# Kernel optimization log

Measured on AMD Instinct MI355X. Metric: run time of the kernel, lower is better.

Reference implementation:

```python
import jax, jax.numpy as jnp
import numpy as np

B, C, D_MODEL, N_HEADS = 2, 2048, 1024, 16


def rotary_matrix(context_length: int, d: int) -> jnp.ndarray:
    """Faithful vectorization of get_rotary_matrix: theta = 10000^(-2*(i-1)/d)."""
    half = d // 2
    i = jnp.arange(half, dtype=jnp.float32)
    theta = 10000.0 ** (-2.0 * (i - 1.0) / d)          # note the (i-1), as in source
    m = jnp.arange(context_length, dtype=jnp.float32)
    ang = m[:, None] * theta                            # [C, d/2]
    c, s = jnp.cos(ang), jnp.sin(ang)
    ev = 2 * jnp.arange(half)
    od = ev + 1
    R = jnp.zeros((context_length, d, d), jnp.float32)
    R = R.at[:, ev, ev].set(c)
    R = R.at[:, ev, od].set(-s)
    R = R.at[:, od, ev].set(s)
    R = R.at[:, od, od].set(c)
    return R


def setup_inputs() -> dict:
    key = jax.random.key(0)
    k1, k2, k3, k4 = jax.random.split(key, 4)
    x = jax.random.normal(k1, (B, C, D_MODEL), dtype=jnp.float32)
    w_qkv = jax.random.normal(k2, (3 * D_MODEL, D_MODEL), dtype=jnp.float32) * 0.02
    w_out = jax.random.normal(k3, (D_MODEL, D_MODEL), dtype=jnp.float32) * 0.02
    b_out = jax.random.normal(k4, (D_MODEL,), dtype=jnp.float32) * 0.02
    return {"x": x, "w_qkv": w_qkv, "w_out": w_out, "b_out": b_out}


def reference(x, w_qkv, w_out, b_out):
    b, c, d = x.shape
    h = N_HEADS
    dh = d // h
    qkv = x @ w_qkv.T                                   # [B,C,3D]
    q, k, v = jnp.split(qkv, 3, axis=-1)
    # [B,C,D] -> [B,H,C,dh]
    q = q.reshape(b, c, h, dh).transpose(0, 2, 1, 3)
    k = k.reshape(b, c, h, dh).transpose(0, 2, 1, 3)
    v = v.reshape(b, c, h, dh).transpose(0, 2, 1, 3)
    R = rotary_matrix(c, dh)                            # [C,dh,dh]
    q_rot = jnp.einsum('bhci,cij->bhcj', q, R)
    k_rot = jnp.einsum('bhci,cij->bhcj', k, R)
    scale = jnp.sqrt(jnp.float32(dh))
    # exact math of the source: exp with no max subtraction, separate num/den
    attn_num = jnp.exp(jnp.einsum('bhqd,bhkd->bhqk', q_rot, k_rot) / scale)
    attn_den = jnp.exp(jnp.einsum('bhqd,bhkd->bhqk', q, k) / scale)
    attn_den = jnp.sum(attn_den, axis=-1, keepdims=True)
    attn = attn_num / attn_den
    causal = jnp.tril(jnp.ones((c, c), jnp.float32))[None, None]
    attn = jnp.where(causal == 0, 0.0, attn)
    y = jnp.einsum('bhqk,bhkd->bhqd', attn, v)
    y = y.transpose(0, 2, 1, 3).reshape(b, c, d)
    return y @ w_out.T + b_out
```

## Files before the change

kernel.cpp:

```cpp
#include <hip/hip_runtime.h>
#include <math.h>
#include <stdint.h>

#define BB 2
#define CC 2048
#define DD 1024
#define HH 16
#define DHH 64
#define HALF 32

typedef __attribute__((ext_vector_type(8))) short bf16x8;
typedef __attribute__((ext_vector_type(4))) float f32x4;
typedef unsigned int u32;

#define EXPC 0.1803368801f

__device__ __forceinline__ ushort f2bf(float f) {
    uint32_t u = __builtin_bit_cast(uint32_t, f);
    u = (u + 0x7FFFu + ((u >> 16) & 1u)) >> 16;
    return (ushort)u;
}

__device__ __forceinline__ void gload16(const void* g, void* lds) {
    __builtin_amdgcn_global_load_lds(
        (const u32 __attribute__((address_space(1)))*)g,
        (u32 __attribute__((address_space(3)))*)lds, 16, 0, 0);
}

__global__ __launch_bounds__(256) void cast3_k(const float* __restrict__ x,
                                               const float* __restrict__ wq,
                                               const float* __restrict__ wo,
                                               ushort* __restrict__ xb,
                                               ushort* __restrict__ wqb,
                                               ushort* __restrict__ wob) {
    int id = blockIdx.x * 256 + threadIdx.x;
    const float* s;
    ushort* d;
    int off;
    if (id < 524288)       { s = x;  d = xb;  off = id; }
    else if (id < 917504)  { s = wq; d = wqb; off = id - 524288; }
    else                   { s = wo; d = wob; off = id - 917504; }
    float4 a = *reinterpret_cast<const float4*>(s + (size_t)off * 8);
    float4 b = *reinterpret_cast<const float4*>(s + (size_t)off * 8 + 4);
    bf16x8 o;
    o[0] = (short)f2bf(a.x); o[1] = (short)f2bf(a.y);
    o[2] = (short)f2bf(a.z); o[3] = (short)f2bf(a.w);
    o[4] = (short)f2bf(b.x); o[5] = (short)f2bf(b.y);
    o[6] = (short)f2bf(b.z); o[7] = (short)f2bf(b.w);
    *reinterpret_cast<bf16x8*>(d + (size_t)off * 8) = o;
}

__global__ __launch_bounds__(256) void rope_table_k(float* __restrict__ ct, float* __restrict__ st) {
    int idx = blockIdx.x * 256 + threadIdx.x;
    if (idx >= CC * HALF) return;
    int m = idx >> 5;
    int t = idx & 31;
    double theta_d = pow(10000.0, -2.0 * ((double)t - 1.0) / 64.0);
    float theta = (float)theta_d;
    float ang = (float)m * theta;
    ct[idx] = cosf(ang);
    st[idx] = sinf(ang);
}

__global__ __launch_bounds__(256) void qkv_gemm_mfma_k(const ushort* __restrict__ xb,
                                                       const ushort* __restrict__ wqb,
                                                       const float* __restrict__ ct,
                                                       const float* __restrict__ st,
                                                       ushort* __restrict__ q,
                                                       ushort* __restrict__ k,
                                                       ushort* __restrict__ qr,
                                                       ushort* __restrict__ kr,
                                                       ushort* __restrict__ vT3) {
    __shared__ ushort Al[128 * 64];
    __shared__ ushort Bl[128 * 64];
    const int tid = threadIdx.x;
    const int w = tid >> 6, l = tid & 63;
    const int l15 = l & 15, lg = l >> 4;
    const int wr = w >> 1, wc = w & 1;
    const int m0 = blockIdx.x * 128, n0 = blockIdx.y * 128;
    const int lrow = l >> 3, lch = l & 7;

    f32x4 acc[4][4];
#pragma unroll
    for (int i = 0; i < 4; i++)
#pragma unroll
        for (int j = 0; j < 4; j++) acc[i][j] = (f32x4){0.f, 0.f, 0.f, 0.f};

    for (int k0 = 0; k0 < 1024; k0 += 64) {
        __syncthreads();
#pragma unroll
        for (int c = 0; c < 4; c++) {
            int row = w * 32 + c * 8 + lrow;
            int gch = (lch ^ (row & 7)) * 8;
            gload16(xb + (size_t)(m0 + row) * 1024 + k0 + gch, &Al[(w * 32 + c * 8) * 64]);
            gload16(wqb + (size_t)(n0 + row) * 1024 + k0 + gch, &Bl[(w * 32 + c * 8) * 64]);
        }
        __syncthreads();
#pragma unroll
        for (int kk = 0; kk < 2; kk++) {
            bf16x8 a[4], b[4];
#pragma unroll
            for (int mt = 0; mt < 4; mt++) {
                int row = wr * 64 + mt * 16 + l15;
                a[mt] = *reinterpret_cast<const bf16x8*>(&Al[row * 64 + ((kk * 4 + lg) ^ (row & 7)) * 8]);
            }
#pragma unroll
            for (int nt = 0; nt < 4; nt++) {
                int row = wc * 64 + nt * 16 + l15;
                b[nt] = *reinterpret_cast<const bf16x8*>(&Bl[row * 64 + ((kk * 4 + lg) ^ (row & 7)) * 8]);
            }
#pragma unroll
            for (int mt = 0; mt < 4; mt++)
#pragma unroll
                for (int nt = 0; nt < 4; nt++)
                    acc[mt][nt] = __builtin_amdgcn_mfma_f32_16x16x32_bf16(a[mt], b[nt], acc[mt][nt], 0, 0, 0);
        }
    }
#pragma unroll
    for (int mt = 0; mt < 4; mt++)
#pragma unroll
        for (int nt = 0; nt < 4; nt++) {
            int n = n0 + wc * 64 + nt * 16 + l15;
            int part = n >> 10;
            int d = n & 1023;
            int h = d >> 6, dd = d & 63;
            int mbase = m0 + wr * 64 + mt * 16 + lg * 4;
            int bb = mbase >> 11, cpos = mbase & 2047;
            if (part == 2) {
                int kt = cpos >> 6, kcol = cpos & 63;
                ushort4 pk;
                pk.x = f2bf(acc[mt][nt][0]); pk.y = f2bf(acc[mt][nt][1]);
                pk.z = f2bf(acc[mt][nt][2]); pk.w = f2bf(acc[mt][nt][3]);
                size_t off = ((((size_t)(bb * HH + h)) * 32 + kt) * 64 + dd) * 64 + kcol;
                *reinterpret_cast<ushort4*>(vT3 + off) = pk;
            } else {
                ushort* dstu = (part == 0) ? q : k;
                ushort* dstr = (part == 0) ? qr : kr;
                const float sgn = (dd & 1) ? -1.f : 1.f;
                const int t = dd >> 1;
#pragma unroll
                for (int r = 0; r < 4; r++) {
                    float val = acc[mt][nt][r];
                    float par = __shfl_xor(val, 1, 64);
                    float c = ct[(cpos + r) * 32 + t];
                    float s = st[(cpos + r) * 32 + t];
                    float rot = val * c + sgn * par * s;
                    size_t base = (((size_t)bb * HH + h) * CC + (cpos + r)) * DHH + dd;
                    dstu[base] = f2bf(val);
                    dstr[base] = f2bf(rot);
                }
            }
        }
}

__global__ __launch_bounds__(256, 2) void attn_fused_k(const ushort* __restrict__ vT3,
                                                       const ushort* __restrict__ qg,
                                                       const ushort* __restrict__ kg,
                                                       const ushort* __restrict__ qrg,
                                                       const ushort* __restrict__ krg,
                                                       ushort* __restrict__ y) {
    __shared__ ushort Kl[2][64 * 64];
    __shared__ ushort Krl[2][64 * 64];
    __shared__ ushort PlA[4][16 * 64];
    __shared__ ushort PlB[4][16 * 64];

    const int tid = threadIdx.x;
    const int w = tid >> 6, l = tid & 63;
    const int l15 = l & 15, lg = l >> 4;
    const int lrow = l >> 3, lch = l & 7;

    const int bid = blockIdx.x;
    const int xcd = bid & 7;
    const int idx = bid >> 3;
    const int sub = idx & 3;
    const int tp = idx >> 2;
    const int bh = xcd * 4 + sub;
    const int NB = 31 - tp;
    const int q0a = tp * 64;
    const int q0b = NB * 64;

    const ushort* qb  = qg  + (size_t)bh * CC * DHH;
    const ushort* kb  = kg  + (size_t)bh * CC * DHH;
    const ushort* qrb = qrg + (size_t)bh * CC * DHH;
    const ushort* krb = krg + (size_t)bh * CC * DHH;
    const ushort* vtb = vT3 + (size_t)bh * 32 * 64 * 64;

    bf16x8 qfA[2], qfB[2], qrfA[2], qrfB[2];
#pragma unroll
    for (int kk = 0; kk < 2; kk++) {
        int ra = q0a + w * 16 + l15;
        int rb = q0b + w * 16 + l15;
        qfA[kk]  = *reinterpret_cast<const bf16x8*>(qb  + (size_t)ra * DHH + kk * 32 + lg * 8);
        qfB[kk]  = *reinterpret_cast<const bf16x8*>(qb  + (size_t)rb * DHH + kk * 32 + lg * 8);
        qrfA[kk] = *reinterpret_cast<const bf16x8*>(qrb + (size_t)ra * DHH + kk * 32 + lg * 8);
        qrfB[kk] = *reinterpret_cast<const bf16x8*>(qrb + (size_t)rb * DHH + kk * 32 + lg * 8);
    }

    f32x4 yaccA[4], yaccB[4];
#pragma unroll
    for (int nt = 0; nt < 4; nt++) {
        yaccA[nt] = (f32x4){0.f, 0.f, 0.f, 0.f};
        yaccB[nt] = (f32x4){0.f, 0.f, 0.f, 0.f};
    }
    float daccA = 0.f, daccB = 0.f;

#define STAGE(KT, BUF)                                                                         \
    {                                                                                          \
        const int sk0 = (KT) * 64;                                                             \
        _Pragma("unroll")                                                                      \
        for (int c = 0; c < 2; c++) {                                                          \
            int row = w * 16 + c * 8 + lrow;                                                   \
            int gch = (lch ^ (row & 7)) * 8;                                                   \
            gload16(kb + (size_t)(sk0 + row) * DHH + gch, &Kl[BUF][(w * 16 + c * 8) * 64]);    \
            if ((KT) <= NB)                                                                    \
                gload16(krb + (size_t)(sk0 + row) * DHH + gch, &Krl[BUF][(w * 16 + c * 8) * 64]); \
        }                                                                                      \
    }

    STAGE(0, 0);
    __syncthreads();
    int cur = 0;

    for (int kt = 0; kt < 32; kt++) {
        if (kt + 1 < 32) STAGE(kt + 1, cur ^ 1);

#pragma unroll
        for (int nt = 0; nt < 4; nt++) {
            bf16x8 ka0, ka1;
            {
                int krow = nt * 16 + l15;
                ka0 = *reinterpret_cast<const bf16x8*>(&Kl[cur][krow * 64 + ((0 + lg) ^ (krow & 7)) * 8]);
                ka1 = *reinterpret_cast<const bf16x8*>(&Kl[cur][krow * 64 + ((4 + lg) ^ (krow & 7)) * 8]);
            }
            f32x4 sA = (f32x4){0.f, 0.f, 0.f, 0.f};
            sA = __builtin_amdgcn_mfma_f32_16x16x32_bf16(ka0, qfA[0], sA, 0, 0, 0);
            sA = __builtin_amdgcn_mfma_f32_16x16x32_bf16(ka1, qfA[1], sA, 0, 0, 0);
            f32x4 sB = (f32x4){0.f, 0.f, 0.f, 0.f};
            sB = __builtin_amdgcn_mfma_f32_16x16x32_bf16(ka0, qfB[0], sB, 0, 0, 0);
            sB = __builtin_amdgcn_mfma_f32_16x16x32_bf16(ka1, qfB[1], sB, 0, 0, 0);
#pragma unroll
            for (int r = 0; r < 4; r++) {
                daccA += __builtin_amdgcn_exp2f(sA[r] * EXPC);
                daccB += __builtin_amdgcn_exp2f(sB[r] * EXPC);
            }
        }

        const bool actA = (kt <= tp);
        const bool actB = (kt <= NB);
        if (actB) {
            const bool diagA = (kt == tp);
            const bool diagB = (kt == NB);
            const int qrowA = q0a + w * 16 + l15;
            const int qrowB = q0b + w * 16 + l15;
#pragma unroll
            for (int nt = 0; nt < 4; nt++) {
                bf16x8 kra0, kra1;
                {
                    int krow = nt * 16 + l15;
                    kra0 = *reinterpret_cast<const bf16x8*>(&Krl[cur][krow * 64 + ((0 + lg) ^ (krow & 7)) * 8]);
                    kra1 = *reinterpret_cast<const bf16x8*>(&Krl[cur][krow * 64 + ((4 + lg) ^ (krow & 7)) * 8]);
                }
                f32x4 sB2 = (f32x4){0.f, 0.f, 0.f, 0.f};
                sB2 = __builtin_amdgcn_mfma_f32_16x16x32_bf16(kra0, qrfB[0], sB2, 0, 0, 0);
                sB2 = __builtin_amdgcn_mfma_f32_16x16x32_bf16(kra1, qrfB[1], sB2, 0, 0, 0);
                float peB[4];
#pragma unroll
                for (int r = 0; r < 4; r++)
                    peB[r] = __builtin_amdgcn_exp2f(sB2[r] * EXPC);
                if (diagB) {
#pragma unroll
                    for (int r = 0; r < 4; r++) {
                        int key = kt * 64 + nt * 16 + lg * 4 + r;
                        peB[r] = (key <= qrowB) ? peB[r] : 0.f;
                    }
                }
                u32 pk0, pk1;
                asm("v_cvt_pk_bf16_f32 %0, %1, %2" : "=v"(pk0) : "v"(peB[0]), "v"(peB[1]));
                asm("v_cvt_pk_bf16_f32 %0, %1, %2" : "=v"(pk1) : "v"(peB[2]), "v"(peB[3]));
                int swzc = (nt * 2 + (lg >> 1)) ^ (l15 & 7);
                uint2 pr; pr.x = pk0; pr.y = pk1;
                *reinterpret_cast<uint2*>(&PlB[w][l15 * 64 + swzc * 8 + (lg & 1) * 4]) = pr;

                if (actA) {
                    f32x4 sA2 = (f32x4){0.f, 0.f, 0.f, 0.f};
                    sA2 = __builtin_amdgcn_mfma_f32_16x16x32_bf16(kra0, qrfA[0], sA2, 0, 0, 0);
                    sA2 = __builtin_amdgcn_mfma_f32_16x16x32_bf16(kra1, qrfA[1], sA2, 0, 0, 0);
                    float peA[4];
#pragma unroll
                    for (int r = 0; r < 4; r++)
                        peA[r] = __builtin_amdgcn_exp2f(sA2[r] * EXPC);
                    if (diagA) {
#pragma unroll
                        for (int r = 0; r < 4; r++) {
                            int key = kt * 64 + nt * 16 + lg * 4 + r;
                            peA[r] = (key <= qrowA) ? peA[r] : 0.f;
                        }
                    }
                    u32 qk0, qk1;
                    asm("v_cvt_pk_bf16_f32 %0, %1, %2" : "=v"(qk0) : "v"(peA[0]), "v"(peA[1]));
                    asm("v_cvt_pk_bf16_f32 %0, %1, %2" : "=v"(qk1) : "v"(peA[2]), "v"(peA[3]));
                    uint2 qr2; qr2.x = qk0; qr2.y = qk1;
                    *reinterpret_cast<uint2*>(&PlA[w][l15 * 64 + swzc * 8 + (lg & 1) * 4]) = qr2;
                }
            }
            bf16x8 paB[2], paA[2];
#pragma unroll
            for (int kk2 = 0; kk2 < 2; kk2++) {
                int rc = (kk2 * 4 + lg) ^ (l15 & 7);
                paB[kk2] = *reinterpret_cast<const bf16x8*>(&PlB[w][l15 * 64 + rc * 8]);
                if (actA)
                    paA[kk2] = *reinterpret_cast<const bf16x8*>(&PlA[w][l15 * 64 + rc * 8]);
            }
            const ushort* vt0 = vtb + (size_t)kt * 64 * 64;
#pragma unroll
            for (int nt2 = 0; nt2 < 4; nt2++) {
                bf16x8 vf0 = *reinterpret_cast<const bf16x8*>(vt0 + (nt2 * 16 + l15) * 64 + lg * 8);
                bf16x8 vf1 = *reinterpret_cast<const bf16x8*>(vt0 + (nt2 * 16 + l15) * 64 + 32 + lg * 8);
                yaccB[nt2] = __builtin_amdgcn_mfma_f32_16x16x32_bf16(paB[0], vf0, yaccB[nt2], 0, 0, 0);
                yaccB[nt2] = __builtin_amdgcn_mfma_f32_16x16x32_bf16(paB[1], vf1, yaccB[nt2], 0, 0, 0);
                if (actA) {
                    yaccA[nt2] = __builtin_amdgcn_mfma_f32_16x16x32_bf16(paA[0], vf0, yaccA[nt2], 0, 0, 0);
                    yaccA[nt2] = __builtin_amdgcn_mfma_f32_16x16x32_bf16(paA[1], vf1, yaccA[nt2], 0, 0, 0);
                }
            }
        }
        __syncthreads();
        cur ^= 1;
    }

    float denA = daccA, denB = daccB;
    denA += __shfl_xor(denA, 16, 64);
    denA += __shfl_xor(denA, 32, 64);
    denB += __shfl_xor(denB, 16, 64);
    denB += __shfl_xor(denB, 32, 64);

    const int b = bh >> 4, h = bh & 15;
#pragma unroll
    for (int r = 0; r < 4; r++) {
        float drA = __shfl(denA, lg * 4 + r, 64);
        float drB = __shfl(denB, lg * 4 + r, 64);
        float invA = 1.f / drA;
        float invB = 1.f / drB;
        int rowA = q0a + w * 16 + lg * 4 + r;
        int rowB = q0b + w * 16 + lg * 4 + r;
#pragma unroll
        for (int nt2 = 0; nt2 < 4; nt2++) {
            y[((size_t)b * CC + rowA) * DD + h * DHH + nt2 * 16 + l15] = f2bf(yaccA[nt2][r] * invA);
            y[((size_t)b * CC + rowB) * DD + h * DHH + nt2 * 16 + l15] = f2bf(yaccB[nt2][r] * invB);
        }
    }
#undef STAGE
}

__global__ __launch_bounds__(256) void out_proj_mfma_k(const ushort* __restrict__ yb,
                                                       const ushort* __restrict__ wob,
                                                       const float* __restrict__ bias,
                                                       float* __restrict__ out) {
    __shared__ ushort Al[128 * 64];
    __shared__ ushort Bl[128 * 64];
    const int tid = threadIdx.x;
    const int w = tid >> 6, l = tid & 63;
    const int l15 = l & 15, lg = l >> 4;
    const int wr = w >> 1, wc = w & 1;
    const int m0 = blockIdx.x * 128, n0 = blockIdx.y * 128;
    const int lrow = l >> 3, lch = l & 7;

    f32x4 acc[4][4];
#pragma unroll
    for (int i = 0; i < 4; i++)
#pragma unroll
        for (int j = 0; j < 4; j++) acc[i][j] = (f32x4){0.f, 0.f, 0.f, 0.f};

    for (int k0 = 0; k0 < 1024; k0 += 64) {
        __syncthreads();
#pragma unroll
        for (int c = 0; c < 4; c++) {
            int row = w * 32 + c * 8 + lrow;
            int gch = (lch ^ (row & 7)) * 8;
            gload16(yb + (size_t)(m0 + row) * 1024 + k0 + gch, &Al[(w * 32 + c * 8) * 64]);
            gload16(wob + (size_t)(n0 + row) * 1024 + k0 + gch, &Bl[(w * 32 + c * 8) * 64]);
        }
        __syncthreads();
#pragma unroll
        for (int kk = 0; kk < 2; kk++) {
            bf16x8 a[4], b[4];
#pragma unroll
            for (int mt = 0; mt < 4; mt++) {
                int row = wr * 64 + mt * 16 + l15;
                a[mt] = *reinterpret_cast<const bf16x8*>(&Al[row * 64 + ((kk * 4 + lg) ^ (row & 7)) * 8]);
            }
#pragma unroll
            for (int nt = 0; nt < 4; nt++) {
                int row = wc * 64 + nt * 16 + l15;
                b[nt] = *reinterpret_cast<const bf16x8*>(&Bl[row * 64 + ((kk * 4 + lg) ^ (row & 7)) * 8]);
            }
#pragma unroll
            for (int mt = 0; mt < 4; mt++)
#pragma unroll
                for (int nt = 0; nt < 4; nt++)
                    acc[mt][nt] = __builtin_amdgcn_mfma_f32_16x16x32_bf16(a[mt], b[nt], acc[mt][nt], 0, 0, 0);
        }
    }
#pragma unroll
    for (int mt = 0; mt < 4; mt++)
#pragma unroll
        for (int nt = 0; nt < 4; nt++) {
            int n = n0 + wc * 64 + nt * 16 + l15;
            float bv = bias[n];
#pragma unroll
            for (int r = 0; r < 4; r++) {
                int m = m0 + wr * 64 + mt * 16 + lg * 4 + r;
                out[(size_t)m * 1024 + n] = acc[mt][nt][r] + bv;
            }
        }
}

extern "C" void kernel_launch(void* const* d_in, const int* in_sizes, int n_in,
                              void* d_out, int out_size, void* d_ws, size_t ws_size,
                              hipStream_t stream) {
    (void)in_sizes; (void)n_in; (void)out_size; (void)ws_size;
    const float* x     = (const float*)d_in[0];
    const float* w_qkv = (const float*)d_in[1];
    const float* w_out = (const float*)d_in[2];
    const float* b_out = (const float*)d_in[3];
    float* out = (float*)d_out;

    char* p = (char*)d_ws;
    float* ct = (float*)p;  p += (size_t)CC * HALF * 4;
    float* st = (float*)p;  p += (size_t)CC * HALF * 4;
    ushort* xb  = (ushort*)p; p += (size_t)4096 * 1024 * 2;
    ushort* wqb = (ushort*)p; p += (size_t)3072 * 1024 * 2;
    ushort* wob = (ushort*)p; p += (size_t)1024 * 1024 * 2;
    const size_t TEN = (size_t)BB * HH * CC * DHH;
    ushort* qb = (ushort*)p; p += TEN * 2;
    ushort* kb = (ushort*)p; p += TEN * 2;
    ushort* vT = (ushort*)p; p += TEN * 2;
    ushort* qr = (ushort*)p; p += TEN * 2;
    ushort* kr = (ushort*)p; p += TEN * 2;
    ushort* yb = (ushort*)p; p += (size_t)4096 * 1024 * 2;

    cast3_k<<<dim3(4096), dim3(256), 0, stream>>>(x, w_qkv, w_out, xb, wqb, wob);
    rope_table_k<<<dim3((CC * HALF) / 256), dim3(256), 0, stream>>>(ct, st);
    qkv_gemm_mfma_k<<<dim3(32, 24), dim3(256), 0, stream>>>(xb, wqb, ct, st, qb, kb, qr, kr, vT);
    attn_fused_k<<<dim3(512), dim3(256), 0, stream>>>(vT, qb, kb, qr, kr, yb);
    out_proj_mfma_k<<<dim3(32, 8), dim3(256), 0, stream>>>(yb, wob, b_out, out);
}
```

Before: 171.6 us.

## Merge rope table into cast kernel and reschedule attention loop MFMAs

```diff
diff --git a/kernel.cpp b/kernel.cpp
--- a/kernel.cpp
+++ b/kernel.cpp
@@ -27,12 +27,25 @@
         (u32 __attribute__((address_space(3)))*)lds, 16, 0, 0);
 }
 
-__global__ __launch_bounds__(256) void cast3_k(const float* __restrict__ x,
-                                               const float* __restrict__ wq,
-                                               const float* __restrict__ wo,
-                                               ushort* __restrict__ xb,
-                                               ushort* __restrict__ wqb,
-                                               ushort* __restrict__ wob) {
+__global__ __launch_bounds__(256) void cast3_rope_k(const float* __restrict__ x,
+                                                    const float* __restrict__ wq,
+                                                    const float* __restrict__ wo,
+                                                    ushort* __restrict__ xb,
+                                                    ushort* __restrict__ wqb,
+                                                    ushort* __restrict__ wob,
+                                                    float* __restrict__ ct,
+                                                    float* __restrict__ st) {
+    if (blockIdx.x >= 4096) {
+        int idx = (blockIdx.x - 4096) * 256 + threadIdx.x;
+        int m = idx >> 5;
+        int t = idx & 31;
+        double theta_d = pow(10000.0, -2.0 * ((double)t - 1.0) / 64.0);
+        float theta = (float)theta_d;
+        float ang = (float)m * theta;
+        ct[idx] = cosf(ang);
+        st[idx] = sinf(ang);
+        return;
+    }
     int id = blockIdx.x * 256 + threadIdx.x;
     const float* s;
     ushort* d;
@@ -48,18 +61,6 @@
     o[4] = (short)f2bf(b.x); o[5] = (short)f2bf(b.y);
     o[6] = (short)f2bf(b.z); o[7] = (short)f2bf(b.w);
     *reinterpret_cast<bf16x8*>(d + (size_t)off * 8) = o;
-}
-
-__global__ __launch_bounds__(256) void rope_table_k(float* __restrict__ ct, float* __restrict__ st) {
-    int idx = blockIdx.x * 256 + threadIdx.x;
-    if (idx >= CC * HALF) return;
-    int m = idx >> 5;
-    int t = idx & 31;
-    double theta_d = pow(10000.0, -2.0 * ((double)t - 1.0) / 64.0);
-    float theta = (float)theta_d;
-    float ang = (float)m * theta;
-    ct[idx] = cosf(ang);
-    st[idx] = sinf(ang);
 }
 
 __global__ __launch_bounds__(256) void qkv_gemm_mfma_k(const ushort* __restrict__ xb,
@@ -202,7 +203,7 @@
         yaccA[nt] = (f32x4){0.f, 0.f, 0.f, 0.f};
         yaccB[nt] = (f32x4){0.f, 0.f, 0.f, 0.f};
     }
-    float daccA = 0.f, daccB = 0.f;
+    float daccA0 = 0.f, daccA1 = 0.f, daccB0 = 0.f, daccB1 = 0.f;
 
 #define STAGE(KT, BUF)                                                                         \
     {                                                                                          \
@@ -222,6 +223,22 @@
     int cur = 0;
 
     for (int kt = 0; kt < 32; kt++) {
+        const bool actA = (kt <= tp);
+        const bool actB = (kt <= NB);
+        const bool diagA = (kt == tp);
+        const bool diagB = (kt == NB);
+
+        bf16x8 vf[4][2];
+        if (actB) {
+            const ushort* vt0 = vtb + (size_t)kt * 64 * 64;
+#pragma unroll
+            for (int nt2 = 0; nt2 < 4; nt2++)
+#pragma unroll
+                for (int kk2 = 0; kk2 < 2; kk2++)
+                    vf[nt2][kk2] = *reinterpret_cast<const bf16x8*>(
+                        vt0 + (nt2 * 16 + l15) * 64 + kk2 * 32 + lg * 8);
+        }
+
         if (kt + 1 < 32) STAGE(kt + 1, cur ^ 1);
 
 #pragma unroll
@@ -232,24 +249,30 @@
                 ka0 = *reinterpret_cast<const bf16x8*>(&Kl[cur][krow * 64 + ((0 + lg) ^ (krow & 7)) * 8]);
                 ka1 = *reinterpret_cast<const bf16x8*>(&Kl[cur][krow * 64 + ((4 + lg) ^ (krow & 7)) * 8]);
             }
+            __builtin_amdgcn_s_setprio(1);
             f32x4 sA = (f32x4){0.f, 0.f, 0.f, 0.f};
             sA = __builtin_amdgcn_mfma_f32_16x16x32_bf16(ka0, qfA[0], sA, 0, 0, 0);
             sA = __builtin_amdgcn_mfma_f32_16x16x32_bf16(ka1, qfA[1], sA, 0, 0, 0);
             f32x4 sB = (f32x4){0.f, 0.f, 0.f, 0.f};
             sB = __builtin_amdgcn_mfma_f32_16x16x32_bf16(ka0, qfB[0], sB, 0, 0, 0);
             sB = __builtin_amdgcn_mfma_f32_16x16x32_bf16(ka1, qfB[1], sB, 0, 0, 0);
-#pragma unroll
-            for (int r = 0; r < 4; r++) {
-                daccA += __builtin_amdgcn_exp2f(sA[r] * EXPC);
-                daccB += __builtin_amdgcn_exp2f(sB[r] * EXPC);
-            }
-        }
-
-        const bool actA = (kt <= tp);
-        const bool actB = (kt <= NB);
+            __builtin_amdgcn_s_setprio(0);
+            if (nt & 1) {
+#pragma unroll
+                for (int r = 0; r < 4; r++) {
+                    daccA1 += __builtin_amdgcn_exp2f(sA[r] * EXPC);
+                    daccB1 += __builtin_amdgcn_exp2f(sB[r] * EXPC);
+                }
+            } else {
+#pragma unroll
+                for (int r = 0; r < 4; r++) {
+                    daccA0 += __builtin_amdgcn_exp2f(sA[r] * EXPC);
+                    daccB0 += __builtin_amdgcn_exp2f(sB[r] * EXPC);
+                }
+            }
+        }
+
         if (actB) {
-            const bool diagA = (kt == tp);
-            const bool diagB = (kt == NB);
             const int qrowA = q0a + w * 16 + l15;
             const int qrowB = q0b + w * 16 + l15;
 #pragma unroll
@@ -260,9 +283,18 @@
                     kra0 = *reinterpret_cast<const bf16x8*>(&Krl[cur][krow * 64 + ((0 + lg) ^ (krow & 7)) * 8]);
                     kra1 = *reinterpret_cast<const bf16x8*>(&Krl[cur][krow * 64 + ((4 + lg) ^ (krow & 7)) * 8]);
                 }
+                __builtin_amdgcn_s_setprio(1);
                 f32x4 sB2 = (f32x4){0.f, 0.f, 0.f, 0.f};
                 sB2 = __builtin_amdgcn_mfma_f32_16x16x32_bf16(kra0, qrfB[0], sB2, 0, 0, 0);
                 sB2 = __builtin_amdgcn_mfma_f32_16x16x32_bf16(kra1, qrfB[1], sB2, 0, 0, 0);
+                f32x4 sA2 = (f32x4){0.f, 0.f, 0.f, 0.f};
+                if (actA) {
+                    sA2 = __builtin_amdgcn_mfma_f32_16x16x32_bf16(kra0, qrfA[0], sA2, 0, 0, 0);
+                    sA2 = __builtin_amdgcn_mfma_f32_16x16x32_bf16(kra1, qrfA[1], sA2, 0, 0, 0);
+                }
+                __builtin_amdgcn_s_setprio(0);
+
+                int swzc = (nt * 2 + (lg >> 1)) ^ (l15 & 7);
                 float peB[4];
 #pragma unroll
                 for (int r = 0; r < 4; r++)
@@ -274,17 +306,13 @@
                         peB[r] = (key <= qrowB) ? peB[r] : 0.f;
                     }
                 }
-                u32 pk0, pk1;
-                asm("v_cvt_pk_bf16_f32 %0, %1, %2" : "=v"(pk0) : "v"(peB[0]), "v"(peB[1]));
-                asm("v_cvt_pk_bf16_f32 %0, %1, %2" : "=v"(pk1) : "v"(peB[2]), "v"(peB[3]));
-                int swzc = (nt * 2 + (lg >> 1)) ^ (l15 & 7);
-                uint2 pr; pr.x = pk0; pr.y = pk1;
-                *reinterpret_cast<uint2*>(&PlB[w][l15 * 64 + swzc * 8 + (lg & 1) * 4]) = pr;
+                u32 pb0, pb1;
+                asm("v_cvt_pk_bf16_f32 %0, %1, %2" : "=v"(pb0) : "v"(peB[0]), "v"(peB[1]));
+                asm("v_cvt_pk_bf16_f32 %0, %1, %2" : "=v"(pb1) : "v"(peB[2]), "v"(peB[3]));
+                uint2 prB; prB.x = pb0; prB.y = pb1;
+                *reinterpret_cast<uint2*>(&PlB[w][l15 * 64 + swzc * 8 + (lg & 1) * 4]) = prB;
 
                 if (actA) {
-                    f32x4 sA2 = (f32x4){0.f, 0.f, 0.f, 0.f};
-                    sA2 = __builtin_amdgcn_mfma_f32_16x16x32_bf16(kra0, qrfA[0], sA2, 0, 0, 0);
-                    sA2 = __builtin_amdgcn_mfma_f32_16x16x32_bf16(kra1, qrfA[1], sA2, 0, 0, 0);
                     float peA[4];
 #pragma unroll
                     for (int r = 0; r < 4; r++)
@@ -296,13 +324,14 @@
                             peA[r] = (key <= qrowA) ? peA[r] : 0.f;
                         }
                     }
-                    u32 qk0, qk1;
-                    asm("v_cvt_pk_bf16_f32 %0, %1, %2" : "=v"(qk0) : "v"(peA[0]), "v"(peA[1]));
-                    asm("v_cvt_pk_bf16_f32 %0, %1, %2" : "=v"(qk1) : "v"(peA[2]), "v"(peA[3]));
-                    uint2 qr2; qr2.x = qk0; qr2.y = qk1;
-                    *reinterpret_cast<uint2*>(&PlA[w][l15 * 64 + swzc * 8 + (lg & 1) * 4]) = qr2;
-                }
-            }
+                    u32 pa0, pa1;
+                    asm("v_cvt_pk_bf16_f32 %0, %1, %2" : "=v"(pa0) : "v"(peA[0]), "v"(peA[1]));
+                    asm("v_cvt_pk_bf16_f32 %0, %1, %2" : "=v"(pa1) : "v"(peA[2]), "v"(peA[3]));
+                    uint2 prA; prA.x = pa0; prA.y = pa1;
+                    *reinterpret_cast<uint2*>(&PlA[w][l15 * 64 + swzc * 8 + (lg & 1) * 4]) = prA;
+                }
+            }
+
             bf16x8 paB[2], paA[2];
 #pragma unroll
             for (int kk2 = 0; kk2 < 2; kk2++) {
@@ -311,24 +340,24 @@
                 if (actA)
                     paA[kk2] = *reinterpret_cast<const bf16x8*>(&PlA[w][l15 * 64 + rc * 8]);
             }
-            const ushort* vt0 = vtb + (size_t)kt * 64 * 64;
+            __builtin_amdgcn_s_setprio(1);
 #pragma unroll
             for (int nt2 = 0; nt2 < 4; nt2++) {
-                bf16x8 vf0 = *reinterpret_cast<const bf16x8*>(vt0 + (nt2 * 16 + l15) * 64 + lg * 8);
-                bf16x8 vf1 = *reinterpret_cast<const bf16x8*>(vt0 + (nt2 * 16 + l15) * 64 + 32 + lg * 8);
-                yaccB[nt2] = __builtin_amdgcn_mfma_f32_16x16x32_bf16(paB[0], vf0, yaccB[nt2], 0, 0, 0);
-                yaccB[nt2] = __builtin_amdgcn_mfma_f32_16x16x32_bf16(paB[1], vf1, yaccB[nt2], 0, 0, 0);
+                yaccB[nt2] = __builtin_amdgcn_mfma_f32_16x16x32_bf16(paB[0], vf[nt2][0], yaccB[nt2], 0, 0, 0);
+                yaccB[nt2] = __builtin_amdgcn_mfma_f32_16x16x32_bf16(paB[1], vf[nt2][1], yaccB[nt2], 0, 0, 0);
                 if (actA) {
-                    yaccA[nt2] = __builtin_amdgcn_mfma_f32_16x16x32_bf16(paA[0], vf0, yaccA[nt2], 0, 0, 0);
-                    yaccA[nt2] = __builtin_amdgcn_mfma_f32_16x16x32_bf16(paA[1], vf1, yaccA[nt2], 0, 0, 0);
-                }
-            }
-        }
+                    yaccA[nt2] = __builtin_amdgcn_mfma_f32_16x16x32_bf16(paA[0], vf[nt2][0], yaccA[nt2], 0, 0, 0);
+                    yaccA[nt2] = __builtin_amdgcn_mfma_f32_16x16x32_bf16(paA[1], vf[nt2][1], yaccA[nt2], 0, 0, 0);
+                }
+            }
+            __builtin_amdgcn_s_setprio(0);
+        }
+
         __syncthreads();
         cur ^= 1;
     }
 
-    float denA = daccA, denB = daccB;
+    float denA = daccA0 + daccA1, denB = daccB0 + daccB1;
     denA += __shfl_xor(denA, 16, 64);
     denA += __shfl_xor(denA, 32, 64);
     denB += __shfl_xor(denB, 16, 64);
@@ -439,8 +468,7 @@
     ushort* kr = (ushort*)p; p += TEN * 2;
     ushort* yb = (ushort*)p; p += (size_t)4096 * 1024 * 2;
 
-    cast3_k<<<dim3(4096), dim3(256), 0, stream>>>(x, w_qkv, w_out, xb, wqb, wob);
-    rope_table_k<<<dim3((CC * HALF) / 256), dim3(256), 0, stream>>>(ct, st);
+    cast3_rope_k<<<dim3(4352), dim3(256), 0, stream>>>(x, w_qkv, w_out, xb, wqb, wob, ct, st);
     qkv_gemm_mfma_k<<<dim3(32, 24), dim3(256), 0, stream>>>(xb, wqb, ct, st, qb, kb, qr, kr, vT);
     attn_fused_k<<<dim3(512), dim3(256), 0, stream>>>(vT, qb, kb, qr, kr, yb);
     out_proj_mfma_k<<<dim3(32, 8), dim3(256), 0, stream>>>(yb, wob, b_out, out);
```

Result: faster. 160.2 us (-6.7%).
